# Performance work log

Hardware: AMD Instinct MI355X
Metric: run time of the kernel (lower is better)

The kernel has to match this reference:

```python
import jax, jax.numpy as jnp
import numpy as np

B, N, C, H, NH, NC = 4, 2048, 256, 128, 8, 3  # batch, points, in_ch, hidden, heads, classes
DH = H // NH


def setup_inputs() -> dict:
    key = jax.random.key(0)
    ki = iter(jax.random.split(key, 48))
    def w(shape, s=0.05):
        return jax.random.normal(next(ki), shape, jnp.float32) * s
    z = lambda n: jnp.zeros((n,), jnp.float32)
    o = lambda n: jnp.ones((n,), jnp.float32)
    inp = dict(x=jax.random.normal(next(ki), (B, N, C), jnp.float32))
    inp.update(fuse_w1=w((H, C)), fuse_b1=z(H), fuse_w2=w((H, H)), fuse_b2=z(H))
    for l in range(2):
        inp[f'attn{l}_in_w'] = w((3 * H, H)); inp[f'attn{l}_in_b'] = z(3 * H)
        inp[f'attn{l}_out_w'] = w((H, H)); inp[f'attn{l}_out_b'] = z(H)
        inp[f'ffn{l}_w1'] = w((2 * H, H)); inp[f'ffn{l}_b1'] = z(2 * H)
        inp[f'ffn{l}_w2'] = w((H, 2 * H)); inp[f'ffn{l}_b2'] = z(H)
        inp[f'ln{2*l}_g'] = o(H); inp[f'ln{2*l}_b'] = z(H)
        inp[f'ln{2*l+1}_g'] = o(H); inp[f'ln{2*l+1}_b'] = z(H)
    inp.update(out_w1=w((H, H)), out_b1=z(H), out_w2=w((NC, H)), out_b2=z(NC))
    inp.update(det_w1=w((H // 2, H)), det_b1=z(H // 2), det_w2=w((1, H // 2)), det_b2=z(1))
    return inp


def _ln(x, g, b):
    m = jnp.mean(x, axis=-1, keepdims=True)
    v = jnp.mean((x - m) ** 2, axis=-1, keepdims=True)
    return (x - m) * jax.lax.rsqrt(v + 1e-5) * g + b


def _mha(x, in_w, in_b, out_w, out_b):
    # nn.MultiheadAttention (batch_first, self-attn), eval mode (no dropout)
    Bq, Nq, _ = x.shape
    qkv = x @ in_w.T + in_b                          # [B,N,3H]
    q, k, v = jnp.split(qkv, 3, axis=-1)
    q = q.reshape(Bq, Nq, NH, DH)
    k = k.reshape(Bq, Nq, NH, DH)
    v = v.reshape(Bq, Nq, NH, DH)
    s = jnp.einsum('bqhd,bkhd->bhqk', q, k) / jnp.sqrt(jnp.float32(DH))
    a = jax.nn.softmax(s, axis=-1)
    o = jnp.einsum('bhqk,bkhd->bqhd', a, v).reshape(Bq, Nq, H)
    return o @ out_w.T + out_b


def _forward(x, fuse_w1, fuse_b1, fuse_w2, fuse_b2,
             attn0_in_w, attn0_in_b, attn0_out_w, attn0_out_b,
             ffn0_w1, ffn0_b1, ffn0_w2, ffn0_b2, ln0_g, ln0_b, ln1_g, ln1_b,
             attn1_in_w, attn1_in_b, attn1_out_w, attn1_out_b,
             ffn1_w1, ffn1_b1, ffn1_w2, ffn1_b2, ln2_g, ln2_b, ln3_g, ln3_b,
             out_w1, out_b1, out_w2, out_b2, det_w1, det_b1, det_w2, det_b2):
    # feature_fusion (dropout = identity in eval)
    h = jnp.maximum(x @ fuse_w1.T + fuse_b1, 0) @ fuse_w2.T + fuse_b2
    layers = [
        (attn0_in_w, attn0_in_b, attn0_out_w, attn0_out_b, ffn0_w1, ffn0_b1, ffn0_w2, ffn0_b2, ln0_g, ln0_b, ln1_g, ln1_b),
        (attn1_in_w, attn1_in_b, attn1_out_w, attn1_out_b, ffn1_w1, ffn1_b1, ffn1_w2, ffn1_b2, ln2_g, ln2_b, ln3_g, ln3_b),
    ]
    for (iw, ib, ow, ob, f1w, f1b, f2w, f2b, g1, be1, g2, be2) in layers:
        h = _ln(h + _mha(h, iw, ib, ow, ob), g1, be1)
        h = _ln(h + (jnp.maximum(h @ f1w.T + f1b, 0) @ f2w.T + f2b), g2, be2)
    refined_logits = jnp.maximum(h @ out_w1.T + out_b1, 0) @ out_w2.T + out_b2   # [B,N,NC]
    head_prob = jax.nn.sigmoid(jnp.maximum(h @ det_w1.T + det_b1, 0) @ det_w2.T + det_b2)[..., 0]  # [B,N]
    quality = jnp.mean(head_prob, axis=1)                                        # [B]
    return refined_logits, head_prob, quality


def reference(x, fuse_w1, fuse_b1, fuse_w2, fuse_b2,
              attn0_in_w, attn0_in_b, attn0_out_w, attn0_out_b,
              ffn0_w1, ffn0_b1, ffn0_w2, ffn0_b2, ln0_g, ln0_b, ln1_g, ln1_b,
              attn1_in_w, attn1_in_b, attn1_out_w, attn1_out_b,
              ffn1_w1, ffn1_b1, ffn1_w2, ffn1_b2, ln2_g, ln2_b, ln3_g, ln3_b,
              out_w1, out_b1, out_w2, out_b2, det_w1, det_b1, det_w2, det_b2):
    return _forward(x, fuse_w1, fuse_b1, fuse_w2, fuse_b2,
                    attn0_in_w, attn0_in_b, attn0_out_w, attn0_out_b,
                    ffn0_w1, ffn0_b1, ffn0_w2, ffn0_b2, ln0_g, ln0_b, ln1_g, ln1_b,
                    attn1_in_w, attn1_in_b, attn1_out_w, attn1_out_b,
                    ffn1_w1, ffn1_b1, ffn1_w2, ffn1_b2, ln2_g, ln2_b, ln3_g, ln3_b,
                    out_w1, out_b1, out_w2, out_b2, det_w1, det_b1, det_w2, det_b2)
```

## Files before the change

### kernel.cpp

```cpp
#include <hip/hip_runtime.h>
#include <cstddef>

constexpr int Bb  = 4;
constexpr int Nn  = 2048;
constexpr int Cc  = 256;
constexpr int Hh  = 128;
constexpr int NHh = 8;
constexpr int DHh = 16;
constexpr int MTOK = Bb * Nn;
#define LOG2E 1.4426950408889634f

typedef __attribute__((ext_vector_type(8))) short bf16x8;
typedef __attribute__((ext_vector_type(4))) short bf16x4;
typedef __attribute__((ext_vector_type(4))) float f32x4;

__device__ __forceinline__ short f32_to_bf16_rne(float f) {
    union { float f; unsigned int u; } c; c.f = f;
    unsigned int r = c.u + 0x7fffu + ((c.u >> 16) & 1u);
    return (short)(r >> 16);
}
__device__ __forceinline__ float bf16_to_f32(short s) {
    union { float f; unsigned int u; } c; c.u = ((unsigned int)(unsigned short)s) << 16;
    return c.f;
}
__device__ __forceinline__ unsigned pack2_bf16(float a, float b) {
    unsigned r;
    asm("v_cvt_pk_bf16_f32 %0, %1, %2" : "=v"(r) : "v"(a), "v"(b));
    return r;
}

struct CvtJobs {
    const float* src[13];
    short*       dst[13];
    int          off[14];
    float*       qzero;
};

__global__ __launch_bounds__(256) void cvt_kernel(CvtJobs j) {
    const int gid = blockIdx.x * 256 + threadIdx.x;
    if (blockIdx.x == 0 && threadIdx.x < 4) j.qzero[threadIdx.x] = 0.f;
    if (gid >= j.off[13]) return;
    int k = 0;
    #pragma unroll
    for (int i = 0; i < 12; ++i) if (gid >= j.off[i + 1]) k = i + 1;
    const int idx = (gid - j.off[k]) * 4;
    float4 v = *(const float4*)(j.src[k] + idx);
    short o4[4] = { f32_to_bf16_rne(v.x), f32_to_bf16_rne(v.y),
                    f32_to_bf16_rne(v.z), f32_to_bf16_rne(v.w) };
    *(bf16x4*)(j.dst[k] + idx) = *(bf16x4*)o4;
}

__global__ __launch_bounds__(256) void gemm_bf16_kernel(
    const short* __restrict__ X, const short* __restrict__ W,
    const float* __restrict__ bias, short* __restrict__ Yb,
    int M, int N, int K, int relu)
{
    __shared__ short As[64 * 40];
    __shared__ short Bs[64 * 40];

    const int tid  = threadIdx.x;
    const int lane = tid & 63;
    const int wv   = tid >> 6;
    const int col  = lane & 15;
    const int g    = lane >> 4;
    const int m0   = blockIdx.y * 64;
    const int n0   = blockIdx.x * 64;
    const int sr   = tid >> 2;
    const int sc   = (tid & 3) * 8;

    f32x4 acc[4] = {};

    for (int k0 = 0; k0 < K; k0 += 32) {
        __syncthreads();
        *(bf16x8*)&As[sr * 40 + sc] =
            *(const bf16x8*)(X + (size_t)(m0 + sr) * K + k0 + sc);
        *(bf16x8*)&Bs[sr * 40 + sc] =
            *(const bf16x8*)(W + (size_t)(n0 + sr) * K + k0 + sc);
        __syncthreads();

        bf16x8 a = *(bf16x8*)&As[(wv * 16 + col) * 40 + g * 8];
        #pragma unroll
        for (int jj = 0; jj < 4; ++jj) {
            bf16x8 b = *(bf16x8*)&Bs[(jj * 16 + col) * 40 + g * 8];
            acc[jj] = __builtin_amdgcn_mfma_f32_16x16x32_bf16(a, b, acc[jj], 0, 0, 0);
        }
    }

    #pragma unroll
    for (int jj = 0; jj < 4; ++jj) {
        const int cn = n0 + jj * 16 + col;
        const float bb = bias[cn];
        #pragma unroll
        for (int r = 0; r < 4; ++r) {
            const int rm = m0 + wv * 16 + g * 4 + r;
            float v = acc[jj][r] + bb;
            if (relu) v = fmaxf(v, 0.f);
            Yb[(size_t)rm * N + cn] = f32_to_bf16_rne(v);
        }
    }
}

template<int K, int CR, bool DO_LN>
__global__ __launch_bounds__(256) void gemmln_kernel(
    const short* __restrict__ X, const short* __restrict__ W,
    const float* __restrict__ bias,
    float* __restrict__ hf, short* __restrict__ hb,
    const float* __restrict__ gw, const float* __restrict__ bw)
{
    constexpr int ST  = K + 8;
    constexpr int NCH = 128 / CR;
    constexpr int NF  = CR / 32;
    __shared__ short As[32 * ST];
    __shared__ short Ws[CR * ST];
    __shared__ float P[32 * 130];

    const int tid  = threadIdx.x;
    const int lane = tid & 63;
    const int wv   = tid >> 6;
    const int col  = lane & 15;
    const int g    = lane >> 4;
    const int m0   = blockIdx.x * 32;
    const int mst  = (wv & 1) * 16;
    const int cb   = (wv >> 1) * (CR / 2);

    for (int i = tid; i < 32 * (K / 8); i += 256) {
        const int r = i / (K / 8), c = (i % (K / 8)) * 8;
        *(bf16x8*)&As[r * ST + c] = *(const bf16x8*)(X + (size_t)(m0 + r) * K + c);
    }

    f32x4 ya[NCH][NF] = {};
    #pragma unroll
    for (int ch = 0; ch < NCH; ++ch) {
        for (int i = tid; i < CR * (K / 8); i += 256) {
            const int r = i / (K / 8), c = (i % (K / 8)) * 8;
            *(bf16x8*)&Ws[r * ST + c] =
                *(const bf16x8*)(W + (size_t)(ch * CR + r) * K + c);
        }
        __syncthreads();
        #pragma unroll
        for (int k0 = 0; k0 < K; k0 += 32) {
            bf16x8 a = *(bf16x8*)&As[(mst + col) * ST + k0 + g * 8];
            #pragma unroll
            for (int f = 0; f < NF; ++f) {
                bf16x8 b = *(bf16x8*)&Ws[(cb + f * 16 + col) * ST + k0 + g * 8];
                ya[ch][f] = __builtin_amdgcn_mfma_f32_16x16x32_bf16(a, b, ya[ch][f], 0, 0, 0);
            }
        }
        __syncthreads();
    }

    #pragma unroll
    for (int ch = 0; ch < NCH; ++ch)
        #pragma unroll
        for (int f = 0; f < NF; ++f) {
            const int cn = ch * CR + cb + f * 16 + col;
            const float bb = bias[cn];
            #pragma unroll
            for (int r = 0; r < 4; ++r)
                P[(mst + g * 4 + r) * 130 + cn] = ya[ch][f][r] + bb;
        }
    __syncthreads();

    #pragma unroll
    for (int rr = 0; rr < 8; ++rr) {
        const int row = wv * 8 + rr;
        const size_t t = m0 + row;
        float2 pv = *(float2*)&P[row * 130 + 2 * lane];
        if (DO_LN) {
            float2 hv = ((const float2*)(hf + t * Hh))[lane];
            float a0 = hv.x + pv.x, a1 = hv.y + pv.y;
            float sum = a0 + a1;
            #pragma unroll
            for (int off = 32; off > 0; off >>= 1) sum += __shfl_xor(sum, off);
            const float mean = sum * (1.f / 128.f);
            const float d0 = a0 - mean, d1 = a1 - mean;
            float vs = d0 * d0 + d1 * d1;
            #pragma unroll
            for (int off = 32; off > 0; off >>= 1) vs += __shfl_xor(vs, off);
            const float rstd = rsqrtf(vs * (1.f / 128.f) + 1e-5f);
            float2 gv = ((const float2*)gw)[lane];
            float2 bv = ((const float2*)bw)[lane];
            float2 r = { d0 * rstd * gv.x + bv.x, d1 * rstd * gv.y + bv.y };
            ((float2*)(hf + t * Hh))[lane] = r;
            *(unsigned*)&hb[t * Hh + lane * 2] = pack2_bf16(r.x, r.y);
        } else {
            ((float2*)(hf + t * Hh))[lane] = pv;
            *(unsigned*)&hb[t * Hh + lane * 2] = pack2_bf16(pv.x, pv.y);
        }
    }
}

template<int K, int MID, int CR1, int CR2, bool DO_LN>
__global__ __launch_bounds__(256) void mlp2_kernel(
    const short* __restrict__ X,
    const short* __restrict__ W1, const float* __restrict__ b1,
    const short* __restrict__ W2, const float* __restrict__ b2,
    float* __restrict__ hf, short* __restrict__ hb,
    const float* __restrict__ gw, const float* __restrict__ bw)
{
    constexpr int STA = K + 8;
    constexpr int STU = MID + 8;
    constexpr int WS1 = CR1 * STA;
    constexpr int WS2 = CR2 * STU;
    constexpr int WSZ = (WS1 > WS2) ? WS1 : WS2;
    __shared__ short As[32 * STA];
    __shared__ short Ws[WSZ];
    __shared__ short U[32 * STU];
    __shared__ float P[32 * 130];

    const int tid  = threadIdx.x;
    const int lane = tid & 63;
    const int wv   = tid >> 6;
    const int col  = lane & 15;
    const int g    = lane >> 4;
    const int m0   = blockIdx.x * 32;
    const int mst  = (wv & 1) * 16;

    for (int i = tid; i < 32 * (K / 8); i += 256) {
        const int r = i / (K / 8), c = (i % (K / 8)) * 8;
        *(bf16x8*)&As[r * STA + c] = *(const bf16x8*)(X + (size_t)(m0 + r) * K + c);
    }

    constexpr int NCH1 = MID / CR1;
    constexpr int NF1  = CR1 / 32;
    const int cb1 = (wv >> 1) * (CR1 / 2);
    #pragma unroll
    for (int ch = 0; ch < NCH1; ++ch) {
        for (int i = tid; i < CR1 * (K / 8); i += 256) {
            const int r = i / (K / 8), c = (i % (K / 8)) * 8;
            *(bf16x8*)&Ws[r * STA + c] =
                *(const bf16x8*)(W1 + (size_t)(ch * CR1 + r) * K + c);
        }
        __syncthreads();
        f32x4 ya[NF1] = {};
        #pragma unroll
        for (int k0 = 0; k0 < K; k0 += 32) {
            bf16x8 a = *(bf16x8*)&As[(mst + col) * STA + k0 + g * 8];
            #pragma unroll
            for (int f = 0; f < NF1; ++f) {
                bf16x8 b = *(bf16x8*)&Ws[(cb1 + f * 16 + col) * STA + k0 + g * 8];
                ya[f] = __builtin_amdgcn_mfma_f32_16x16x32_bf16(a, b, ya[f], 0, 0, 0);
            }
        }
        #pragma unroll
        for (int f = 0; f < NF1; ++f) {
            const int cn = ch * CR1 + cb1 + f * 16 + col;
            const float bb = b1[cn];
            #pragma unroll
            for (int r = 0; r < 4; ++r)
                U[(mst + g * 4 + r) * STU + cn] =
                    f32_to_bf16_rne(fmaxf(ya[f][r] + bb, 0.f));
        }
        __syncthreads();
    }

    constexpr int NCH2 = 128 / CR2;
    constexpr int NF2  = CR2 / 32;
    const int cb2 = (wv >> 1) * (CR2 / 2);
    f32x4 yb[NCH2][NF2] = {};
    #pragma unroll
    for (int ch = 0; ch < NCH2; ++ch) {
        for (int i = tid; i < CR2 * (MID / 8); i += 256) {
            const int r = i / (MID / 8), c = (i % (MID / 8)) * 8;
            *(bf16x8*)&Ws[r * STU + c] =
                *(const bf16x8*)(W2 + (size_t)(ch * CR2 + r) * MID + c);
        }
        __syncthreads();
        #pragma unroll
        for (int k0 = 0; k0 < MID; k0 += 32) {
            bf16x8 a = *(bf16x8*)&U[(mst + col) * STU + k0 + g * 8];
            #pragma unroll
            for (int f = 0; f < NF2; ++f) {
                bf16x8 b = *(bf16x8*)&Ws[(cb2 + f * 16 + col) * STU + k0 + g * 8];
                yb[ch][f] = __builtin_amdgcn_mfma_f32_16x16x32_bf16(a, b, yb[ch][f], 0, 0, 0);
            }
        }
        __syncthreads();
    }

    #pragma unroll
    for (int ch = 0; ch < NCH2; ++ch)
        #pragma unroll
        for (int f = 0; f < NF2; ++f) {
            const int cn = ch * CR2 + cb2 + f * 16 + col;
            const float bb = b2[cn];
            #pragma unroll
            for (int r = 0; r < 4; ++r)
                P[(mst + g * 4 + r) * 130 + cn] = yb[ch][f][r] + bb;
        }
    __syncthreads();

    #pragma unroll
    for (int rr = 0; rr < 8; ++rr) {
        const int row = wv * 8 + rr;
        const size_t t = m0 + row;
        float2 pv = *(float2*)&P[row * 130 + 2 * lane];
        if (DO_LN) {
            float2 hv = ((const float2*)(hf + t * Hh))[lane];
            float a0 = hv.x + pv.x, a1 = hv.y + pv.y;
            float sum = a0 + a1;
            #pragma unroll
            for (int off = 32; off > 0; off >>= 1) sum += __shfl_xor(sum, off);
            const float mean = sum * (1.f / 128.f);
            const float d0 = a0 - mean, d1 = a1 - mean;
            float vs = d0 * d0 + d1 * d1;
            #pragma unroll
            for (int off = 32; off > 0; off >>= 1) vs += __shfl_xor(vs, off);
            const float rstd = rsqrtf(vs * (1.f / 128.f) + 1e-5f);
            float2 gv = ((const float2*)gw)[lane];
            float2 bv = ((const float2*)bw)[lane];
            float2 r = { d0 * rstd * gv.x + bv.x, d1 * rstd * gv.y + bv.y };
            ((float2*)(hf + t * Hh))[lane] = r;
            *(unsigned*)&hb[t * Hh + lane * 2] = pack2_bf16(r.x, r.y);
        } else {
            ((float2*)(hf + t * Hh))[lane] = pv;
            *(unsigned*)&hb[t * Hh + lane * 2] = pack2_bf16(pv.x, pv.y);
        }
    }
}

__global__ __launch_bounds__(256) void head_kernel(
    const short* __restrict__ X,
    const short* __restrict__ W1b, const float* __restrict__ b1,
    const short* __restrict__ DW1b, const float* __restrict__ db1,
    const float* __restrict__ w2, const float* __restrict__ b2,
    const float* __restrict__ dw2, const float* __restrict__ db2,
    float* __restrict__ out)
{
    constexpr int K = 128, ST = K + 8;
    __shared__ short As[32 * ST];
    __shared__ short Ws[64 * ST];
    __shared__ float P[32 * 196];

    const int tid  = threadIdx.x;
    const int lane = tid & 63;
    const int wv   = tid >> 6;
    const int col  = lane & 15;
    const int g    = lane >> 4;
    const int m0   = blockIdx.x * 32;
    const int mst  = (wv & 1) * 16;
    const int cb   = (wv >> 1) * 32;

    for (int i = tid; i < 32 * (K / 8); i += 256) {
        const int r = i / (K / 8), c = (i % (K / 8)) * 8;
        *(bf16x8*)&As[r * ST + c] = *(const bf16x8*)(X + (size_t)(m0 + r) * K + c);
    }

    f32x4 ya[3][2] = {};
    #pragma unroll
    for (int ch = 0; ch < 3; ++ch) {
        for (int i = tid; i < 64 * (K / 8); i += 256) {
            const int r = i / (K / 8), c = (i % (K / 8)) * 8;
            const int rg = ch * 64 + r;
            const short* src = (rg < 128) ? (W1b + (size_t)rg * K)
                                          : (DW1b + (size_t)(rg - 128) * K);
            *(bf16x8*)&Ws[r * ST + c] = *(const bf16x8*)(src + c);
        }
        __syncthreads();
        #pragma unroll
        for (int k0 = 0; k0 < K; k0 += 32) {
            bf16x8 a = *(bf16x8*)&As[(mst + col) * ST + k0 + g * 8];
            #pragma unroll
            for (int f = 0; f < 2; ++f) {
                bf16x8 b = *(bf16x8*)&Ws[(cb + f * 16 + col) * ST + k0 + g * 8];
                ya[ch][f] = __builtin_amdgcn_mfma_f32_16x16x32_bf16(a, b, ya[ch][f], 0, 0, 0);
            }
        }
        __syncthreads();
    }

    #pragma unroll
    for (int ch = 0; ch < 3; ++ch)
        #pragma unroll
        for (int f = 0; f < 2; ++f) {
            const int cn = ch * 64 + cb + f * 16 + col;
            const float bb = (cn < 128) ? b1[cn] : db1[cn - 128];
            #pragma unroll
            for (int r = 0; r < 4; ++r)
                P[(mst + g * 4 + r) * 196 + cn] = fmaxf(ya[ch][f][r] + bb, 0.f);
        }
    __syncthreads();

    const float w20 = w2[2 * lane],       w21 = w2[2 * lane + 1];
    const float w22 = w2[128 + 2 * lane], w23 = w2[129 + 2 * lane];
    const float w24 = w2[256 + 2 * lane], w25 = w2[257 + 2 * lane];
    const float dwl = dw2[lane];
    float qacc = 0.f;
    #pragma unroll
    for (int rr = 0; rr < 8; ++rr) {
        const int row = wv * 8 + rr;
        const size_t t = m0 + row;
        const float x0 = P[row * 196 + 2 * lane];
        const float x1 = P[row * 196 + 2 * lane + 1];
        float s0 = x0 * w20 + x1 * w21;
        float s1 = x0 * w22 + x1 * w23;
        float s2 = x0 * w24 + x1 * w25;
        float d  = P[row * 196 + 128 + lane] * dwl;
        #pragma unroll
        for (int off = 32; off > 0; off >>= 1) {
            s0 += __shfl_xor(s0, off);
            s1 += __shfl_xor(s1, off);
            s2 += __shfl_xor(s2, off);
            d  += __shfl_xor(d,  off);
        }
        if (lane == 0) {
            out[t * 3 + 0] = s0 + b2[0];
            out[t * 3 + 1] = s1 + b2[1];
            out[t * 3 + 2] = s2 + b2[2];
            const float prob = 1.f / (1.f + __expf(-(d + db2[0])));
            out[24576 + t] = prob;
            qacc += prob;
        }
    }
    if (lane == 0)
        atomicAdd(&out[32768 + (m0 >> 11)], qacc * (1.f / (float)Nn));
}

constexpr int KT = 128;
constexpr int KS = 28;
constexpr int VS = 132;

__global__ __launch_bounds__(256) void attn_kernel(
    const short* __restrict__ qkv, short* __restrict__ out)
{
    __shared__ short Ks[KT * KS];
    __shared__ short Vs[DHh * VS];

    const int tid  = threadIdx.x;
    const int lane = tid & 63;
    const int wv   = tid >> 6;
    const int col  = lane & 15;
    const int g    = lane >> 4;
    const int hd   = blockIdx.y;
    const int b    = blockIdx.z;
    const int q0   = blockIdx.x * 64 + wv * 16;

    const short* base = qkv + (size_t)b * Nn * 384;

    bf16x8 qf = {};
    if (g < 2) {
        bf16x8 qraw = *(const bf16x8*)(base + (size_t)(q0 + col) * 384 + hd * DHh + g * 8);
        const float qs = 0.25f * LOG2E;
        #pragma unroll
        for (int i = 0; i < 8; ++i)
            qf[i] = f32_to_bf16_rne(bf16_to_f32(qraw[i]) * qs);
    }

    f32x4 o    = {0.f, 0.f, 0.f, 0.f};
    f32x4 lacc = {0.f, 0.f, 0.f, 0.f};
    const short one_bf16 = (short)0x3F80;
    const bf16x8 ones = { one_bf16, one_bf16, one_bf16, one_bf16,
                          one_bf16, one_bf16, one_bf16, one_bf16 };

    const int ksr = tid >> 1;
    const int ksd = (tid & 1) * 8;
    const int va  = tid >> 2;
    const int vd  = (tid & 3) * 4;

    const short* kptr = base + (size_t)ksr * 384 + Hh + hd * DHh + ksd;
    const short* vptr = base + (size_t)(2 * va) * 384 + 2 * Hh + hd * DHh + vd;
    bf16x8 kreg = *(const bf16x8*)kptr;
    bf16x4 vr0  = *(const bf16x4*)vptr;
    bf16x4 vr1  = *(const bf16x4*)(vptr + 384);

    for (int kt = 0; kt < Nn; kt += KT) {
        __syncthreads();

        *(bf16x8*)&Ks[ksr * KS + ksd] = kreg;
        {
            unsigned a0 = ((const unsigned*)&vr0)[0], a1 = ((const unsigned*)&vr0)[1];
            unsigned b0 = ((const unsigned*)&vr1)[0], b1 = ((const unsigned*)&vr1)[1];
            *(unsigned*)&Vs[(vd + 0) * VS + 2 * va] = __builtin_amdgcn_perm(b0, a0, 0x05040100);
            *(unsigned*)&Vs[(vd + 1) * VS + 2 * va] = __builtin_amdgcn_perm(b0, a0, 0x07060302);
            *(unsigned*)&Vs[(vd + 2) * VS + 2 * va] = __builtin_amdgcn_perm(b1, a1, 0x05040100);
            *(unsigned*)&Vs[(vd + 3) * VS + 2 * va] = __builtin_amdgcn_perm(b1, a1, 0x07060302);
        }

        if (kt + KT < Nn) {
            kptr += KT * 384;
            vptr += KT * 384;
            kreg = *(const bf16x8*)kptr;
            vr0  = *(const bf16x4*)vptr;
            vr1  = *(const bf16x4*)(vptr + 384);
        }

        asm volatile("s_waitcnt lgkmcnt(0)" ::: "memory");
        __builtin_amdgcn_s_barrier();

        #pragma unroll
        for (int s = 0; s < 4; ++s) {
            bf16x8 kf0 = {}, kf1 = {};
            if (g < 2) {
                kf0 = *(bf16x8*)&Ks[(s * 32 + col) * KS + g * 8];
                kf1 = *(bf16x8*)&Ks[(s * 32 + 16 + col) * KS + g * 8];
            }
            f32x4 z = {0.f, 0.f, 0.f, 0.f};
            f32x4 sA = __builtin_amdgcn_mfma_f32_16x16x32_bf16(kf0, qf, z, 0, 0, 0);
            f32x4 sB = __builtin_amdgcn_mfma_f32_16x16x32_bf16(kf1, qf, z, 0, 0, 0);

            union { bf16x8 v; unsigned u[4]; } pf;
            pf.u[0] = pack2_bf16(__builtin_amdgcn_exp2f(sA[0]),
                                 __builtin_amdgcn_exp2f(sA[1]));
            pf.u[1] = pack2_bf16(__builtin_amdgcn_exp2f(sA[2]),
                                 __builtin_amdgcn_exp2f(sA[3]));
            pf.u[2] = pack2_bf16(__builtin_amdgcn_exp2f(sB[0]),
                                 __builtin_amdgcn_exp2f(sB[1]));
            pf.u[3] = pack2_bf16(__builtin_amdgcn_exp2f(sB[2]),
                                 __builtin_amdgcn_exp2f(sB[3]));

            bf16x8 vf;
            ((bf16x4*)&vf)[0] = *(bf16x4*)&Vs[col * VS + s * 32 + g * 4];
            ((bf16x4*)&vf)[1] = *(bf16x4*)&Vs[col * VS + s * 32 + 16 + g * 4];

            o    = __builtin_amdgcn_mfma_f32_16x16x32_bf16(pf.v, vf,   o,    0, 0, 0);
            lacc = __builtin_amdgcn_mfma_f32_16x16x32_bf16(pf.v, ones, lacc, 0, 0, 0);
        }
    }

    #pragma unroll
    for (int r = 0; r < 4; ++r) {
        const float inv = __builtin_amdgcn_rcpf(lacc[r]);
        out[(size_t)(b * Nn + q0 + g * 4 + r) * Hh + hd * DHh + col] =
            f32_to_bf16_rne(o[r] * inv);
    }
}

extern "C" void kernel_launch(void* const* d_in, const int* in_sizes, int n_in,
                              void* d_out, int out_size, void* d_ws, size_t ws_size,
                              hipStream_t stream)
{
    char* W8 = (char*)d_ws;
    float* hf   = (float*)(W8 + 0);
    short* hb   = (short*)(W8 + 4194304);
    short* wb   = (short*)(W8 + 6291456);
    char*  regA = W8 + 7340032;
    char*  regB = W8 + 13631488;

    short* xb    = (short*)regA;
    short* qkvb  = (short*)regA;
    short* attno = (short*)regB;
    float* out   = (float*)d_out;

    const int wsz[12]  = {32768,16384,49152,16384,32768,32768,49152,16384,32768,32768,16384,8192};
    const int wsrc[12] = {1, 3, 5, 7, 9, 11, 17, 19, 21, 23, 29, 33};
    int woff[13]; woff[0] = 0;
    for (int i = 0; i < 12; ++i) woff[i + 1] = woff[i] + wsz[i];

    CvtJobs jobs;
    int acc = 0;
    for (int i = 0; i < 12; ++i) {
        jobs.src[i] = (const float*)d_in[wsrc[i]];
        jobs.dst[i] = wb + woff[i];
        jobs.off[i] = acc;
        acc += wsz[i] / 4;
    }
    jobs.src[12] = (const float*)d_in[0];
    jobs.dst[12] = xb;
    jobs.off[12] = acc;
    acc += (MTOK * Cc) / 4;
    jobs.off[13] = acc;
    jobs.qzero = out + 32768;

    hipLaunchKernelGGL(cvt_kernel, dim3((acc + 255) / 256), dim3(256), 0, stream, jobs);

    hipLaunchKernelGGL((mlp2_kernel<256, 128, 32, 64, false>), dim3(MTOK / 32), dim3(256), 0,
                       stream, xb, wb + woff[0], (const float*)d_in[2],
                       wb + woff[1], (const float*)d_in[4], hf, hb, nullptr, nullptr);

    for (int l = 0; l < 2; ++l) {
        const int ib = 5 + l * 12;
        const int wbase = 2 + l * 4;
        hipLaunchKernelGGL(gemm_bf16_kernel, dim3(384 / 64, MTOK / 64), dim3(256), 0, stream,
                           hb, wb + woff[wbase + 0], (const float*)d_in[ib + 1], qkvb,
                           MTOK, 3 * Hh, Hh, 0);
        hipLaunchKernelGGL(attn_kernel, dim3(Nn / 64, NHh, Bb), dim3(256), 0, stream,
                           qkvb, attno);
        hipLaunchKernelGGL((gemmln_kernel<128, 64, true>), dim3(MTOK / 32), dim3(256), 0, stream,
                           attno, wb + woff[wbase + 1], (const float*)d_in[ib + 3],
                           hf, hb, (const float*)d_in[ib + 8], (const float*)d_in[ib + 9]);
        hipLaunchKernelGGL((mlp2_kernel<128, 256, 64, 32, true>), dim3(MTOK / 32), dim3(256), 0,
                           stream, hb, wb + woff[wbase + 2], (const float*)d_in[ib + 5],
                           wb + woff[wbase + 3], (const float*)d_in[ib + 7],
                           hf, hb, (const float*)d_in[ib + 10], (const float*)d_in[ib + 11]);
    }

    hipLaunchKernelGGL(head_kernel, dim3(MTOK / 32), dim3(256), 0, stream,
                       hb, wb + woff[10], (const float*)d_in[30],
                       wb + woff[11], (const float*)d_in[34],
                       (const float*)d_in[31], (const float*)d_in[32],
                       (const float*)d_in[35], (const float*)d_in[36], out);
}
```

Measured before the change: 293.1 us.

## Split attention key range across two block halves and merge partials in LDS

Doubles the attention block to 512 threads; each group of four waves processes half of the key sequence with its own K/V LDS buffers. The second half writes its unnormalized output and row-sum accumulators to shared memory, and the first half adds them before normalizing and storing. This halves the serial key loop per wave to expose more parallelism and latency hiding. In exchange it uses more LDS, adds a final barrier and exchange, and may reduce resident blocks per CU.

After: 321.7 us. +9.8%, slower.

```diff
diff --git a/kernel.cpp b/kernel.cpp
--- a/kernel.cpp
+++ b/kernel.cpp
@@ -420,20 +420,23 @@
 constexpr int KS = 28;
 constexpr int VS = 132;
 
-__global__ __launch_bounds__(256) void attn_kernel(
+__global__ __launch_bounds__(512) void attn_kernel(
     const short* __restrict__ qkv, short* __restrict__ out)
 {
-    __shared__ short Ks[KT * KS];
-    __shared__ short Vs[DHh * VS];
+    __shared__ short Ks[2][KT * KS];
+    __shared__ short Vs[2][DHh * VS];
+    __shared__ float ExO[4][256];
+    __shared__ float ExL[4][256];
 
     const int tid  = threadIdx.x;
     const int lane = tid & 63;
     const int wv   = tid >> 6;
+    const int half = wv >> 2;
     const int col  = lane & 15;
     const int g    = lane >> 4;
     const int hd   = blockIdx.y;
     const int b    = blockIdx.z;
-    const int q0   = blockIdx.x * 64 + wv * 16;
+    const int q0   = blockIdx.x * 64 + (wv & 3) * 16;
 
     const short* base = qkv + (size_t)b * Nn * 384;
 
@@ -452,31 +455,36 @@
     const bf16x8 ones = { one_bf16, one_bf16, one_bf16, one_bf16,
                           one_bf16, one_bf16, one_bf16, one_bf16 };
 
-    const int ksr = tid >> 1;
-    const int ksd = (tid & 1) * 8;
-    const int va  = tid >> 2;
-    const int vd  = (tid & 3) * 4;
-
-    const short* kptr = base + (size_t)ksr * 384 + Hh + hd * DHh + ksd;
-    const short* vptr = base + (size_t)(2 * va) * 384 + 2 * Hh + hd * DHh + vd;
+    const int htid = tid & 255;
+    const int ksr = htid >> 1;
+    const int ksd = (htid & 1) * 8;
+    const int va  = htid >> 2;
+    const int vd  = (htid & 3) * 4;
+    const int kbase = half * (Nn / 2);
+
+    short* ks = Ks[half];
+    short* vs = Vs[half];
+
+    const short* kptr = base + (size_t)(kbase + ksr) * 384 + Hh + hd * DHh + ksd;
+    const short* vptr = base + (size_t)(kbase + 2 * va) * 384 + 2 * Hh + hd * DHh + vd;
     bf16x8 kreg = *(const bf16x8*)kptr;
     bf16x4 vr0  = *(const bf16x4*)vptr;
     bf16x4 vr1  = *(const bf16x4*)(vptr + 384);
 
-    for (int kt = 0; kt < Nn; kt += KT) {
-        __syncthreads();
-
-        *(bf16x8*)&Ks[ksr * KS + ksd] = kreg;
+    for (int kt = 0; kt < Nn / 2; kt += KT) {
+        __syncthreads();
+
+        *(bf16x8*)&ks[ksr * KS + ksd] = kreg;
         {
             unsigned a0 = ((const unsigned*)&vr0)[0], a1 = ((const unsigned*)&vr0)[1];
             unsigned b0 = ((const unsigned*)&vr1)[0], b1 = ((const unsigned*)&vr1)[1];
-            *(unsigned*)&Vs[(vd + 0) * VS + 2 * va] = __builtin_amdgcn_perm(b0, a0, 0x05040100);
-            *(unsigned*)&Vs[(vd + 1) * VS + 2 * va] = __builtin_amdgcn_perm(b0, a0, 0x07060302);
-            *(unsigned*)&Vs[(vd + 2) * VS + 2 * va] = __builtin_amdgcn_perm(b1, a1, 0x05040100);
-            *(unsigned*)&Vs[(vd + 3) * VS + 2 * va] = __builtin_amdgcn_perm(b1, a1, 0x07060302);
-        }
-
-        if (kt + KT < Nn) {
+            *(unsigned*)&vs[(vd + 0) * VS + 2 * va] = __builtin_amdgcn_perm(b0, a0, 0x05040100);
+            *(unsigned*)&vs[(vd + 1) * VS + 2 * va] = __builtin_amdgcn_perm(b0, a0, 0x07060302);
+            *(unsigned*)&vs[(vd + 2) * VS + 2 * va] = __builtin_amdgcn_perm(b1, a1, 0x05040100);
+            *(unsigned*)&vs[(vd + 3) * VS + 2 * va] = __builtin_amdgcn_perm(b1, a1, 0x07060302);
+        }
+
+        if (kt + KT < Nn / 2) {
             kptr += KT * 384;
             vptr += KT * 384;
             kreg = *(const bf16x8*)kptr;
@@ -491,8 +499,8 @@
         for (int s = 0; s < 4; ++s) {
             bf16x8 kf0 = {}, kf1 = {};
             if (g < 2) {
-                kf0 = *(bf16x8*)&Ks[(s * 32 + col) * KS + g * 8];
-                kf1 = *(bf16x8*)&Ks[(s * 32 + 16 + col) * KS + g * 8];
+                kf0 = *(bf16x8*)&ks[(s * 32 + col) * KS + g * 8];
+                kf1 = *(bf16x8*)&ks[(s * 32 + 16 + col) * KS + g * 8];
             }
             f32x4 z = {0.f, 0.f, 0.f, 0.f};
             f32x4 sA = __builtin_amdgcn_mfma_f32_16x16x32_bf16(kf0, qf, z, 0, 0, 0);
@@ -509,19 +517,32 @@
                                  __builtin_amdgcn_exp2f(sB[3]));
 
             bf16x8 vf;
-            ((bf16x4*)&vf)[0] = *(bf16x4*)&Vs[col * VS + s * 32 + g * 4];
-            ((bf16x4*)&vf)[1] = *(bf16x4*)&Vs[col * VS + s * 32 + 16 + g * 4];
+            ((bf16x4*)&vf)[0] = *(bf16x4*)&vs[col * VS + s * 32 + g * 4];
+            ((bf16x4*)&vf)[1] = *(bf16x4*)&vs[col * VS + s * 32 + 16 + g * 4];
 
             o    = __builtin_amdgcn_mfma_f32_16x16x32_bf16(pf.v, vf,   o,    0, 0, 0);
             lacc = __builtin_amdgcn_mfma_f32_16x16x32_bf16(pf.v, ones, lacc, 0, 0, 0);
         }
     }
 
-    #pragma unroll
-    for (int r = 0; r < 4; ++r) {
-        const float inv = __builtin_amdgcn_rcpf(lacc[r]);
-        out[(size_t)(b * Nn + q0 + g * 4 + r) * Hh + hd * DHh + col] =
-            f32_to_bf16_rne(o[r] * inv);
+    if (half == 1) {
+        const int w = wv & 3;
+        #pragma unroll
+        for (int r = 0; r < 4; ++r) {
+            ExO[w][(g * 4 + r) * 16 + col] = o[r];
+            ExL[w][(g * 4 + r) * 16 + col] = lacc[r];
+        }
+    }
+    __syncthreads();
+    if (half == 0) {
+        #pragma unroll
+        for (int r = 0; r < 4; ++r) {
+            const float ov = o[r]    + ExO[wv][(g * 4 + r) * 16 + col];
+            const float lv = lacc[r] + ExL[wv][(g * 4 + r) * 16 + col];
+            const float inv = __builtin_amdgcn_rcpf(lv);
+            out[(size_t)(b * Nn + q0 + g * 4 + r) * Hh + hd * DHh + col] =
+                f32_to_bf16_rne(ov * inv);
+        }
     }
 }
 
@@ -573,7 +594,7 @@
         hipLaunchKernelGGL(gemm_bf16_kernel, dim3(384 / 64, MTOK / 64), dim3(256), 0, stream,
                            hb, wb + woff[wbase + 0], (const float*)d_in[ib + 1], qkvb,
                            MTOK, 3 * Hh, Hh, 0);
-        hipLaunchKernelGGL(attn_kernel, dim3(Nn / 64, NHh, Bb), dim3(256), 0, stream,
+        hipLaunchKernelGGL(attn_kernel, dim3(Nn / 64, NHh, Bb), dim3(512), 0, stream,
                            qkvb, attno);
         hipLaunchKernelGGL((gemmln_kernel<128, 64, true>), dim3(MTOK / 32), dim3(256), 0, stream,
                            attno, wb + woff[wbase + 1], (const float*)d_in[ib + 3],
```
